# Kernel optimization log

Measured on AMD Instinct MI355X. Metric: run time of the kernel, lower is better.

The kernel has to match this reference:

```python
import jax, jax.numpy as jnp
import numpy as np

T, D, R, C, L = 4096, 512, 32, 32, 2  # time, input, trace, context, num_blocks
NEG_SLOPE = 0.01
EPS = 1e-5  # eqx LayerNorm default


def _layernorm(x, g, b):
    m = jnp.mean(x, -1, keepdims=True)
    v = jnp.var(x, -1, keepdims=True)
    return g * (x - m) * jax.lax.rsqrt(v + EPS) + b


def _ffa_scan(a, b, pre, s0, start):
    # a:[R], b:[C], pre:[T,R,C] real>=0, s0:[1,R,C] complex64, start:[T] bool
    ab = jax.lax.complex(jnp.broadcast_to(-jnp.abs(a)[:, None], (R, C)),
                         jnp.broadcast_to(b[None, :], (R, C)))  # log decay+rotation
    ts = jnp.concatenate([jnp.zeros((1,), jnp.float32), jnp.ones((T,), jnp.float32)])
    vals = jnp.concatenate([s0, pre.astype(jnp.complex64)], axis=0)  # [T+1,R,C]
    rst = jnp.concatenate([jnp.zeros((1,), bool), start])

    def op(l, r):
        tl, sl, dl = l
        tr, sr, dr = r
        decay = jnp.exp(ab[None, :, :] * tr[:, None, None])  # gamma^{t_r}
        s = jnp.where(dr[:, None, None], sr, sr + sl * decay)
        t = jnp.where(dr, tr, tl + tr)
        return (t, s, dl | dr)

    _, states, _ = jax.lax.associative_scan(op, (ts, vals, rst))
    return states[1:]  # [T,R,C]


def _forward(x, start_b, state_real, state_imag, Wt, Wc, a, b,
             W0, b0, g0, beta0, W1, b1, g1, beta1):
    h = x
    z = x
    for i in range(L):
        tr = h @ Wt[i].T  # [T,R]
        ct = h @ Wc[i].T  # [T,R] (source maps context proj to trace_size too; R==C)
        pre = jnp.abs(tr[:, :, None] * ct[:, None, :])  # [T,R,C] outer product
        pre = pre / (1e-8 + jnp.sum(pre, axis=(-2, -1), keepdims=True))
        s0 = jax.lax.complex(state_real[i], state_imag[i])  # [1,R,C]
        states = _ffa_scan(a[i], b[i], pre, s0, start_b)
        s = states.reshape(T, R * C)
        mag = jnp.log1p(jnp.abs(s))
        ang = jnp.angle(s)
        scaled = jnp.concatenate([mag * jnp.sin(ang), mag * jnp.cos(ang)], axis=-1)  # [T,2RC]
        z = jax.nn.leaky_relu(_layernorm(scaled @ W0[i].T + b0[i], g0[i], beta0[i]), NEG_SLOPE)
        z = jax.nn.leaky_relu(_layernorm(z @ W1[i].T + b1[i], g1[i], beta1[i]), NEG_SLOPE)
        h = h + z  # residual feeds next block; NSFFM returns last block's z
    return z


def setup_inputs() -> dict:
    key = jax.random.key(0)
    ks = jax.random.split(key, 8)
    x = jax.random.normal(ks[0], (T, D), jnp.float32)
    start = jax.random.randint(ks[1], (T,), 0, 2).astype(jnp.int32)
    next_done = jax.random.randint(ks[2], (T,), 0, 2).astype(jnp.int32)
    Wt = jax.random.normal(ks[3], (L, R, D), jnp.float32) / np.sqrt(D)
    Wc = jax.random.normal(ks[4], (L, R, D), jnp.float32) / np.sqrt(D)
    # ffa.init: a = linspace decays, b = log-spaced angular frequencies
    a = jnp.broadcast_to(jnp.linspace(1e-6, 0.5, R, dtype=jnp.float32)[None], (L, R)).copy()
    b = jnp.broadcast_to((2 * jnp.pi / jnp.exp(jnp.linspace(np.log(1.0), np.log(1024.0), C))).astype(jnp.float32)[None], (L, C)).copy()
    W0 = jax.random.normal(ks[5], (L, D, 2 * R * C), jnp.float32) * 0.01  # default_init scale=0.01
    W1 = jax.random.normal(ks[6], (L, D, D), jnp.float32) / np.sqrt(D)
    return {
        'x': x, 'start': start, 'next_done': next_done,
        'state_real': jnp.zeros((L, 1, R, C), jnp.float32),
        'state_imag': jnp.zeros((L, 1, R, C), jnp.float32),
        'Wt': Wt, 'Wc': Wc, 'a': a, 'b': b,
        'W0': W0, 'b0': jnp.zeros((L, D), jnp.float32),
        'g0': jnp.ones((L, D), jnp.float32), 'beta0': jnp.zeros((L, D), jnp.float32),
        'W1': W1, 'b1': jnp.zeros((L, D), jnp.float32),
        'g1': jnp.ones((L, D), jnp.float32), 'beta1': jnp.zeros((L, D), jnp.float32),
    }


def reference(x, start, next_done, state_real, state_imag, Wt, Wc, a, b,
              W0, b0, g0, beta0, W1, b1, g1, beta1):
    del next_done  # not used in the scan math (kept for interface parity)
    start_b = start.astype(bool)
    return _forward(x, start_b, state_real, state_imag, Wt, Wc, a, b,
                    W0, b0, g0, beta0, W1, b1, g1, beta1)
```

## Files before the change

kernel.cpp:

```cpp
#include <hip/hip_runtime.h>
#include <math.h>

#define TT 4096
#define DD 512
#define RR 32
#define CC 32
#define RC 1024
#define LL 2
#define CHUNK 32
#define NCHUNK 128
#define NEG_SLOPE 0.01f
#define LN_EPS 1e-5f

typedef __attribute__((ext_vector_type(8))) __bf16 bf16x8;
typedef __attribute__((ext_vector_type(4))) float f32x4;

__device__ __forceinline__ unsigned short f2bf(float f) {
    unsigned int u = __builtin_bit_cast(unsigned int, f);
    u += 0x7fffu + ((u >> 16) & 1u);
    return (unsigned short)(u >> 16);
}

#define NX4  524288
#define NW04 524288
#define NW14 131072
__global__ __launch_bounds__(256) void conv_all_kernel(const float4* __restrict__ x,
                                                       const float4* __restrict__ W0,
                                                       const float4* __restrict__ W1,
                                                       ushort4* __restrict__ xb,
                                                       ushort4* __restrict__ W0b,
                                                       ushort4* __restrict__ W1b) {
    int i = blockIdx.x * 256 + threadIdx.x;
    const float4* src; ushort4* dst; int j;
    if (i < NX4) { src = x; dst = xb; j = i; }
    else if (i < NX4 + NW04) { src = W0; dst = W0b; j = i - NX4; }
    else { src = W1; dst = W1b; j = i - NX4 - NW04; }
    float4 v = src[j];
    ushort4 o;
    o.x = f2bf(v.x); o.y = f2bf(v.y); o.z = f2bf(v.z); o.w = f2bf(v.w);
    dst[j] = o;
}

__global__ __launch_bounds__(256) void pack_wtc_kernel(const float* __restrict__ Wt,
                                                       const float* __restrict__ Wc,
                                                       ushort4* __restrict__ Wtc) {
    int i = blockIdx.x * 256 + threadIdx.x;
    int e = i * 4;
    int l = e >> 15;
    int r = (e >> 9) & 63;
    int k = e & 511;
    const float4 v = (r < 32)
        ? *(const float4*)&Wt[((size_t)l * 32 + r) * 512 + k]
        : *(const float4*)&Wc[((size_t)l * 32 + (r - 32)) * 512 + k];
    ushort4 o;
    o.x = f2bf(v.x); o.y = f2bf(v.y); o.z = f2bf(v.z); o.w = f2bf(v.w);
    Wtc[i] = o;
}

__global__ __launch_bounds__(256) void denom_reduce_kernel(const float* __restrict__ tcp,
                                                           float* __restrict__ tcabs) {
    int lrow = threadIdx.x >> 3;
    int q = threadIdx.x & 7;
    int row = blockIdx.x * 32 + lrow;
    size_t base = (size_t)row * 64 + q * 8;
    float v[8];
#pragma unroll
    for (int e = 0; e < 8; ++e) v[e] = 0.f;
#pragma unroll
    for (int z = 0; z < 4; ++z) {
        const float4* p = (const float4*)(tcp + (size_t)z * TT * 64 + base);
        float4 u0 = p[0], u1 = p[1];
        v[0] += u0.x; v[1] += u0.y; v[2] += u0.z; v[3] += u0.w;
        v[4] += u1.x; v[5] += u1.y; v[6] += u1.z; v[7] += u1.w;
    }
    float s = 0.f;
#pragma unroll
    for (int e = 0; e < 8; ++e) { v[e] = fabsf(v[e]); s += v[e]; }
    __shared__ float red[32][8];
    red[lrow][q] = s;
    __syncthreads();
    float str = red[lrow][0] + red[lrow][1] + red[lrow][2] + red[lrow][3];
    float stc = red[lrow][4] + red[lrow][5] + red[lrow][6] + red[lrow][7];
    float inv = 1.f / (1e-8f + str * stc);
    float scale = (q < 4) ? inv : 1.f;
    float4 o0 = make_float4(v[0] * scale, v[1] * scale, v[2] * scale, v[3] * scale);
    float4 o1 = make_float4(v[4] * scale, v[5] * scale, v[6] * scale, v[7] * scale);
    float4* dst = (float4*)(tcabs + base);
    dst[0] = o0; dst[1] = o1;
}

__global__ __launch_bounds__(256) void scan_pass1(const float* __restrict__ tcabs,
                                                  const int* __restrict__ start,
                                                  const float* __restrict__ a,
                                                  const float* __restrict__ b,
                                                  float4* __restrict__ ab4) {
    int tid = blockIdx.x * 256 + threadIdx.x;
    int rc = tid & (RC - 1);
    int chunk = tid >> 10;
    int r = rc >> 5, c = rc & 31;
    float e = expf(-fabsf(a[r]));
    float gr = e * cosf(b[c]);
    float gi = e * sinf(b[c]);
    float alr = 1.f, ali = 0.f, ber = 0.f, bei = 0.f;
    int t0 = chunk * CHUNK;
    for (int j = 0; j < CHUNK; ++j) {
        int t = t0 + j;
        float pre = tcabs[t * 64 + r] * tcabs[t * 64 + 32 + c];
        if (start[t]) {
            alr = 0.f; ali = 0.f; ber = pre; bei = 0.f;
        } else {
            float nbr = pre + gr * ber - gi * bei;
            float nbi =       gr * bei + gi * ber;
            float nar = gr * alr - gi * ali;
            float nai = gr * ali + gi * alr;
            ber = nbr; bei = nbi; alr = nar; ali = nai;
        }
    }
    ab4[chunk * RC + rc] = make_float4(alr, ali, ber, bei);
}

__global__ __launch_bounds__(256) void scan_combine(const float4* __restrict__ ab4,
                                                    const float* __restrict__ s0r,
                                                    const float* __restrict__ s0i,
                                                    float2* __restrict__ inc) {
    int rc = blockIdx.x * 256 + threadIdx.x;
    float sr = s0r[rc], si = s0i[rc];
    for (int kb = 0; kb < NCHUNK; kb += 8) {
        float4 buf[8];
#pragma unroll
        for (int u = 0; u < 8; ++u) buf[u] = ab4[(kb + u) * RC + rc];
#pragma unroll
        for (int u = 0; u < 8; ++u) {
            inc[(kb + u) * RC + rc] = make_float2(sr, si);
            float nsr = buf[u].z + buf[u].x * sr - buf[u].y * si;
            float nsi = buf[u].w + buf[u].x * si + buf[u].y * sr;
            sr = nsr; si = nsi;
        }
    }
}

__global__ __launch_bounds__(256) void scan_pass2(const float* __restrict__ tcabs,
                                                  const int* __restrict__ start,
                                                  const float* __restrict__ a,
                                                  const float* __restrict__ b,
                                                  const float2* __restrict__ inc,
                                                  unsigned short* __restrict__ scaled) {
    int tid = blockIdx.x * 256 + threadIdx.x;
    int rc = tid & (RC - 1);
    int chunk = tid >> 10;
    int r = rc >> 5, c = rc & 31;
    float e = expf(-fabsf(a[r]));
    float gr = e * cosf(b[c]);
    float gi = e * sinf(b[c]);
    float2 s = inc[chunk * RC + rc];
    float sr = s.x, si = s.y;
    int t0 = chunk * CHUNK;
    for (int j = 0; j < CHUNK; ++j) {
        int t = t0 + j;
        float pre = tcabs[t * 64 + r] * tcabs[t * 64 + 32 + c];
        if (start[t]) {
            sr = pre; si = 0.f;
        } else {
            float nsr = pre + gr * sr - gi * si;
            float nsi =       gr * si + gi * sr;
            sr = nsr; si = nsi;
        }
        float m = sqrtf(sr * sr + si * si);
        float mag = log1pf(m);
        float f = (m > 0.f) ? (mag / m) : 0.f;
        scaled[(size_t)t * 2048 + rc]        = f2bf(si * f);
        scaled[(size_t)t * 2048 + 1024 + rc] = f2bf(sr * f);
    }
}

template <int K, int N, int SPLITK>
__global__ __launch_bounds__(256) void gemm_bt_mfma(const unsigned short* __restrict__ A,
                                                    const unsigned short* __restrict__ B,
                                                    float* __restrict__ Cm) {
    __shared__ unsigned short As[128 * 32];
    __shared__ unsigned short Bs[64 * 32];
    const int tid = threadIdx.x;
    const int w = tid >> 6, lane = tid & 63;
    const int bm = blockIdx.y * 128, bn = blockIdx.x * 64;
    const int kbeg = blockIdx.z * (K / SPLITK);
    const int kend = kbeg + (K / SPLITK);
    const int wr = w >> 1, wc = w & 1;
    const int lr = lane >> 2;
    const int sl = lane & 3;
    const int swz_st = sl ^ ((lr >> 1) & 3);
    const size_t a_row0 = (size_t)(bm + w * 16 + lr);
    const size_t a_row1 = (size_t)(bm + 64 + w * 16 + lr);
    const size_t b_row  = (size_t)(bn + w * 16 + lr);
    const unsigned short* gA0 = A + a_row0 * K + sl * 8;
    const unsigned short* gA1 = A + a_row1 * K + sl * 8;
    const unsigned short* gB  = B + b_row  * K + sl * 8;
    const int wA0 = (w * 16 + lr) * 32 + swz_st * 8;
    const int wA1 = (64 + w * 16 + lr) * 32 + swz_st * 8;
    const int wB  = (w * 16 + lr) * 32 + swz_st * 8;
    const int fr = lane & 15;
    const int kslot = (lane >> 4) ^ ((fr >> 1) & 3);
    f32x4 acc[4][2] = {};

    uint4 va0 = *(const uint4*)(gA0 + kbeg);
    uint4 va1 = *(const uint4*)(gA1 + kbeg);
    uint4 vb  = *(const uint4*)(gB  + kbeg);
    for (int k0 = kbeg; k0 < kend; k0 += 32) {
        __syncthreads();
        *(uint4*)&As[wA0] = va0;
        *(uint4*)&As[wA1] = va1;
        *(uint4*)&Bs[wB]  = vb;
        __syncthreads();
        if (k0 + 32 < kend) {
            va0 = *(const uint4*)(gA0 + k0 + 32);
            va1 = *(const uint4*)(gA1 + k0 + 32);
            vb  = *(const uint4*)(gB  + k0 + 32);
        }
        bf16x8 af[4], bfr[2];
#pragma unroll
        for (int mi = 0; mi < 4; ++mi) {
            int row = wr * 64 + mi * 16 + fr;
            af[mi] = *(const bf16x8*)&As[row * 32 + kslot * 8];
        }
#pragma unroll
        for (int ni = 0; ni < 2; ++ni) {
            int row = wc * 32 + ni * 16 + fr;
            bfr[ni] = *(const bf16x8*)&Bs[row * 32 + kslot * 8];
        }
#pragma unroll
        for (int mi = 0; mi < 4; ++mi)
#pragma unroll
            for (int ni = 0; ni < 2; ++ni)
                acc[mi][ni] = __builtin_amdgcn_mfma_f32_16x16x32_bf16(
                    af[mi], bfr[ni], acc[mi][ni], 0, 0, 0);
    }
    float* Cz = Cm + (size_t)blockIdx.z * TT * N;
    const int ccol0 = bn + wc * 32 + fr;
    const int crow0 = bm + wr * 64 + (lane >> 4) * 4;
#pragma unroll
    for (int ni = 0; ni < 2; ++ni) {
        int col = ccol0 + ni * 16;
#pragma unroll
        for (int mi = 0; mi < 4; ++mi)
#pragma unroll
            for (int q = 0; q < 4; ++q)
                Cz[(size_t)(crow0 + mi * 16 + q) * N + col] = acc[mi][ni][q];
    }
}

__global__ __launch_bounds__(256) void ln_lrelu_kernel(const float* __restrict__ y0,
                                                       const float* __restrict__ y1,
                                                       const float* __restrict__ badd,
                                                       const float* __restrict__ g,
                                                       const float* __restrict__ be,
                                                       unsigned short* __restrict__ zb,
                                                       const float* __restrict__ res,
                                                       unsigned short* __restrict__ hbf,
                                                       float* __restrict__ fout) {
    int t = blockIdx.x;
    int tid = threadIdx.x;
    size_t base = (size_t)t * 512;
    float v0 = y0[base + tid] + y1[base + tid] + badd[tid];
    float v1 = y0[base + 256 + tid] + y1[base + 256 + tid] + badd[256 + tid];
    float s = v0 + v1, ss = v0 * v0 + v1 * v1;
#pragma unroll
    for (int o = 32; o > 0; o >>= 1) {
        s  += __shfl_down(s, o);
        ss += __shfl_down(ss, o);
    }
    __shared__ float sh[8];
    __shared__ float mrs[2];
    int wid = tid >> 6, lane = tid & 63;
    if (lane == 0) { sh[wid] = s; sh[4 + wid] = ss; }
    __syncthreads();
    if (tid == 0) {
        float S = sh[0] + sh[1] + sh[2] + sh[3];
        float SS = sh[4] + sh[5] + sh[6] + sh[7];
        float m = S * (1.f / 512.f);
        float var = SS * (1.f / 512.f) - m * m;
        mrs[0] = m;
        mrs[1] = rsqrtf(var + LN_EPS);
    }
    __syncthreads();
    float m = mrs[0], rs = mrs[1];
    float z0 = g[tid] * (v0 - m) * rs + be[tid];
    float z1 = g[256 + tid] * (v1 - m) * rs + be[256 + tid];
    z0 = (z0 > 0.f) ? z0 : NEG_SLOPE * z0;
    z1 = (z1 > 0.f) ? z1 : NEG_SLOPE * z1;
    if (zb)   { zb[base + tid] = f2bf(z0); zb[base + 256 + tid] = f2bf(z1); }
    if (hbf) {
        float h0 = (res ? res[base + tid] : 0.f) + z0;
        float h1 = (res ? res[base + 256 + tid] : 0.f) + z1;
        hbf[base + tid] = f2bf(h0);
        hbf[base + 256 + tid] = f2bf(h1);
    }
    if (fout) { fout[base + tid] = z0; fout[base + 256 + tid] = z1; }
}

extern "C" void kernel_launch(void* const* d_in, const int* in_sizes, int n_in,
                              void* d_out, int out_size, void* d_ws, size_t ws_size,
                              hipStream_t stream) {
    const float* x     = (const float*)d_in[0];
    const int*   start = (const int*)d_in[1];
    const float* s0r = (const float*)d_in[3];
    const float* s0i = (const float*)d_in[4];
    const float* Wt  = (const float*)d_in[5];
    const float* Wc  = (const float*)d_in[6];
    const float* a   = (const float*)d_in[7];
    const float* b   = (const float*)d_in[8];
    const float* W0  = (const float*)d_in[9];
    const float* b0  = (const float*)d_in[10];
    const float* g0  = (const float*)d_in[11];
    const float* be0 = (const float*)d_in[12];
    const float* W1  = (const float*)d_in[13];
    const float* b1  = (const float*)d_in[14];
    const float* g1  = (const float*)d_in[15];
    const float* be1 = (const float*)d_in[16];
    float* out = (float*)d_out;
    float* ws  = (float*)d_ws;

    float* p = ws;
    float* tcp    = p; p += 1048576;
    float* tcabs  = p; p += 262144;
    float4* ab4   = (float4*)p; p += 524288;
    float2* inc   = (float2*)p; p += 262144;
    unsigned short* scaled = (unsigned short*)p; p += 4194304;
    float* ybufp  = p; p += 4194304;
    unsigned short* zbuf_bf = (unsigned short*)p; p += 1048576;
    unsigned short* x_bf    = (unsigned short*)p; p += 1048576;
    unsigned short* h_bf    = (unsigned short*)p; p += 1048576;
    unsigned short* Wtcbf   = (unsigned short*)p; p += 32768;
    unsigned short* W0bf    = (unsigned short*)p; p += 1048576;
    unsigned short* W1bf    = (unsigned short*)p; p += 262144;

    conv_all_kernel<<<(NX4 + NW04 + NW14) / 256, 256, 0, stream>>>(
        (const float4*)x, (const float4*)W0, (const float4*)W1,
        (ushort4*)x_bf, (ushort4*)W0bf, (ushort4*)W1bf);
    pack_wtc_kernel<<<64, 256, 0, stream>>>(Wt, Wc, (ushort4*)Wtcbf);

    for (int i = 0; i < LL; ++i) {
        const unsigned short* hb = (i == 0) ? x_bf : h_bf;
        gemm_bt_mfma<512, 64, 4><<<dim3(1, 32, 4), 256, 0, stream>>>(
            hb, Wtcbf + (size_t)i * 64 * 512, tcp);
        denom_reduce_kernel<<<128, 256, 0, stream>>>(tcp, tcabs);
        scan_pass1<<<NCHUNK * RC / 256, 256, 0, stream>>>(
            tcabs, start, a + i * RR, b + i * CC, ab4);
        scan_combine<<<4, 256, 0, stream>>>(ab4, s0r + i * RC, s0i + i * RC, inc);
        scan_pass2<<<NCHUNK * RC / 256, 256, 0, stream>>>(
            tcabs, start, a + i * RR, b + i * CC, inc, scaled);
        gemm_bt_mfma<2048, 512, 2><<<dim3(8, 32, 2), 256, 0, stream>>>(
            scaled, W0bf + (size_t)i * 512 * 2048, ybufp);
        ln_lrelu_kernel<<<TT, 256, 0, stream>>>(
            ybufp, ybufp + (size_t)TT * 512, b0 + i * DD, g0 + i * DD, be0 + i * DD,
            zbuf_bf, nullptr, nullptr, nullptr);
        gemm_bt_mfma<512, 512, 2><<<dim3(8, 32, 2), 256, 0, stream>>>(
            zbuf_bf, W1bf + (size_t)i * 512 * 512, ybufp);
        ln_lrelu_kernel<<<TT, 256, 0, stream>>>(
            ybufp, ybufp + (size_t)TT * 512, b1 + i * DD, g1 + i * DD, be1 + i * DD,
            nullptr,
            (i < LL - 1) ? x : nullptr,
            (i < LL - 1) ? h_bf : nullptr,
            (i == LL - 1) ? out : nullptr);
    }
}
```

Measured before the change: 214.8 us.

## Fuse projection with denominator, fold scan combine into pass2, widen GEMM K-tile

The two setup conversion kernels become one launch. The projection GEMM now computes the abs and row-normalisation directly in its epilogue, with no split-K and no separate reduce kernel. The serial scan_combine kernel is removed: each pass2 block recomputes its chunk's incoming state by folding all prior chunk summaries, which trades a launch and a serial pass for redundant O(chunk) work per block. The generic GEMM moves from a 32-wide to a 64-wide K tile with a new XOR swizzle, giving fewer barriers per K and more MFMAs per sync.

After: 324.9 us. 51.2% more time.

```diff
diff --git a/kernel.cpp b/kernel.cpp
--- a/kernel.cpp
+++ b/kernel.cpp
@@ -24,69 +24,137 @@
 #define NX4  524288
 #define NW04 524288
 #define NW14 131072
-__global__ __launch_bounds__(256) void conv_all_kernel(const float4* __restrict__ x,
-                                                       const float4* __restrict__ W0,
-                                                       const float4* __restrict__ W1,
-                                                       ushort4* __restrict__ xb,
-                                                       ushort4* __restrict__ W0b,
-                                                       ushort4* __restrict__ W1b) {
+#define NCV  (NX4 + NW04 + NW14)
+#define NPK  16384
+__global__ __launch_bounds__(256) void setup_kernel(const float4* __restrict__ x,
+                                                    const float4* __restrict__ W0,
+                                                    const float4* __restrict__ W1,
+                                                    const float* __restrict__ Wt,
+                                                    const float* __restrict__ Wc,
+                                                    ushort4* __restrict__ xb,
+                                                    ushort4* __restrict__ W0b,
+                                                    ushort4* __restrict__ W1b,
+                                                    ushort4* __restrict__ Wtc) {
     int i = blockIdx.x * 256 + threadIdx.x;
-    const float4* src; ushort4* dst; int j;
-    if (i < NX4) { src = x; dst = xb; j = i; }
-    else if (i < NX4 + NW04) { src = W0; dst = W0b; j = i - NX4; }
-    else { src = W1; dst = W1b; j = i - NX4 - NW04; }
-    float4 v = src[j];
+    float4 v;
+    ushort4* dst;
+    int j;
+    if (i < NCV) {
+        const float4* src;
+        if (i < NX4) { src = x; dst = xb; j = i; }
+        else if (i < NX4 + NW04) { src = W0; dst = W0b; j = i - NX4; }
+        else { src = W1; dst = W1b; j = i - NX4 - NW04; }
+        v = src[j];
+    } else {
+        int ii = i - NCV;
+        if (ii >= NPK) return;
+        int e = ii * 4;
+        int l = e >> 15;
+        int r = (e >> 9) & 63;
+        int k = e & 511;
+        v = (r < 32) ? *(const float4*)&Wt[((size_t)l * 32 + r) * 512 + k]
+                     : *(const float4*)&Wc[((size_t)l * 32 + (r - 32)) * 512 + k];
+        dst = Wtc; j = ii;
+    }
     ushort4 o;
     o.x = f2bf(v.x); o.y = f2bf(v.y); o.z = f2bf(v.z); o.w = f2bf(v.w);
     dst[j] = o;
 }
 
-__global__ __launch_bounds__(256) void pack_wtc_kernel(const float* __restrict__ Wt,
-                                                       const float* __restrict__ Wc,
-                                                       ushort4* __restrict__ Wtc) {
-    int i = blockIdx.x * 256 + threadIdx.x;
-    int e = i * 4;
-    int l = e >> 15;
-    int r = (e >> 9) & 63;
-    int k = e & 511;
-    const float4 v = (r < 32)
-        ? *(const float4*)&Wt[((size_t)l * 32 + r) * 512 + k]
-        : *(const float4*)&Wc[((size_t)l * 32 + (r - 32)) * 512 + k];
-    ushort4 o;
-    o.x = f2bf(v.x); o.y = f2bf(v.y); o.z = f2bf(v.z); o.w = f2bf(v.w);
-    Wtc[i] = o;
-}
-
-__global__ __launch_bounds__(256) void denom_reduce_kernel(const float* __restrict__ tcp,
-                                                           float* __restrict__ tcabs) {
-    int lrow = threadIdx.x >> 3;
-    int q = threadIdx.x & 7;
-    int row = blockIdx.x * 32 + lrow;
-    size_t base = (size_t)row * 64 + q * 8;
-    float v[8];
-#pragma unroll
-    for (int e = 0; e < 8; ++e) v[e] = 0.f;
-#pragma unroll
-    for (int z = 0; z < 4; ++z) {
-        const float4* p = (const float4*)(tcp + (size_t)z * TT * 64 + base);
-        float4 u0 = p[0], u1 = p[1];
-        v[0] += u0.x; v[1] += u0.y; v[2] += u0.z; v[3] += u0.w;
-        v[4] += u1.x; v[5] += u1.y; v[6] += u1.z; v[7] += u1.w;
-    }
-    float s = 0.f;
-#pragma unroll
-    for (int e = 0; e < 8; ++e) { v[e] = fabsf(v[e]); s += v[e]; }
-    __shared__ float red[32][8];
-    red[lrow][q] = s;
+__global__ __launch_bounds__(256) void proj_denom_kernel(const unsigned short* __restrict__ A,
+                                                         const unsigned short* __restrict__ B,
+                                                         float* __restrict__ tcabs) {
+    __shared__ __align__(16) unsigned short As[128 * 64];
+    __shared__ __align__(16) unsigned short Bs[64 * 64];
+    __shared__ float sums[128][2];
+    const int tid = threadIdx.x;
+    const int w = tid >> 6, lane = tid & 63;
+    const int bm = blockIdx.y * 128;
+    const int wr = w >> 1, wc = w & 1;
+    const int fr = lane & 15, hi = lane >> 4;
+    const int K = 512;
+    const unsigned short* ga[4]; int wa[4];
+    const unsigned short* gb[2]; int wb[2];
+#pragma unroll
+    for (int u = 0; u < 4; ++u) {
+        int vid = u * 256 + tid;
+        int row = vid >> 3, k8 = vid & 7;
+        ga[u] = A + (size_t)(bm + row) * K + k8 * 8;
+        wa[u] = row * 64 + ((k8 ^ (row & 7)) * 8);
+    }
+#pragma unroll
+    for (int u = 0; u < 2; ++u) {
+        int vid = u * 256 + tid;
+        int row = vid >> 3, k8 = vid & 7;
+        gb[u] = B + (size_t)row * K + k8 * 8;
+        wb[u] = row * 64 + ((k8 ^ (row & 7)) * 8);
+    }
+    f32x4 acc[4][2] = {};
+    uint4 pa[4], pb[2];
+#pragma unroll
+    for (int u = 0; u < 4; ++u) pa[u] = *(const uint4*)ga[u];
+#pragma unroll
+    for (int u = 0; u < 2; ++u) pb[u] = *(const uint4*)gb[u];
+    for (int k0 = 0; k0 < K; k0 += 64) {
+        __syncthreads();
+#pragma unroll
+        for (int u = 0; u < 4; ++u) *(uint4*)&As[wa[u]] = pa[u];
+#pragma unroll
+        for (int u = 0; u < 2; ++u) *(uint4*)&Bs[wb[u]] = pb[u];
+        __syncthreads();
+        if (k0 + 64 < K) {
+#pragma unroll
+            for (int u = 0; u < 4; ++u) pa[u] = *(const uint4*)(ga[u] + k0 + 64);
+#pragma unroll
+            for (int u = 0; u < 2; ++u) pb[u] = *(const uint4*)(gb[u] + k0 + 64);
+        }
+#pragma unroll
+        for (int kk = 0; kk < 2; ++kk) {
+            const int ks = kk * 4 + hi;
+            bf16x8 af[4], bfv[2];
+#pragma unroll
+            for (int mi = 0; mi < 4; ++mi) {
+                int row = wr * 64 + mi * 16 + fr;
+                af[mi] = *(const bf16x8*)&As[row * 64 + ((ks ^ (row & 7)) * 8)];
+            }
+#pragma unroll
+            for (int ni = 0; ni < 2; ++ni) {
+                int row = wc * 32 + ni * 16 + fr;
+                bfv[ni] = *(const bf16x8*)&Bs[row * 64 + ((ks ^ (row & 7)) * 8)];
+            }
+#pragma unroll
+            for (int mi = 0; mi < 4; ++mi)
+#pragma unroll
+                for (int ni = 0; ni < 2; ++ni)
+                    acc[mi][ni] = __builtin_amdgcn_mfma_f32_16x16x32_bf16(
+                        af[mi], bfv[ni], acc[mi][ni], 0, 0, 0);
+        }
+    }
+#pragma unroll
+    for (int mi = 0; mi < 4; ++mi)
+#pragma unroll
+        for (int q = 0; q < 4; ++q) {
+            float v = fabsf(acc[mi][0][q]) + fabsf(acc[mi][1][q]);
+            v += __shfl_xor(v, 1);
+            v += __shfl_xor(v, 2);
+            v += __shfl_xor(v, 4);
+            v += __shfl_xor(v, 8);
+            if (fr == 0) sums[wr * 64 + mi * 16 + hi * 4 + q][wc] = v;
+        }
     __syncthreads();
-    float str = red[lrow][0] + red[lrow][1] + red[lrow][2] + red[lrow][3];
-    float stc = red[lrow][4] + red[lrow][5] + red[lrow][6] + red[lrow][7];
-    float inv = 1.f / (1e-8f + str * stc);
-    float scale = (q < 4) ? inv : 1.f;
-    float4 o0 = make_float4(v[0] * scale, v[1] * scale, v[2] * scale, v[3] * scale);
-    float4 o1 = make_float4(v[4] * scale, v[5] * scale, v[6] * scale, v[7] * scale);
-    float4* dst = (float4*)(tcabs + base);
-    dst[0] = o0; dst[1] = o1;
+#pragma unroll
+    for (int mi = 0; mi < 4; ++mi)
+#pragma unroll
+        for (int q = 0; q < 4; ++q) {
+            int rl = wr * 64 + mi * 16 + hi * 4 + q;
+            float inv = 1.f / (1e-8f + sums[rl][0] * sums[rl][1]);
+            float scale = (wc == 0) ? inv : 1.f;
+#pragma unroll
+            for (int ni = 0; ni < 2; ++ni) {
+                int col = wc * 32 + ni * 16 + fr;
+                tcabs[(size_t)(bm + rl) * 64 + col] = fabsf(acc[mi][ni][q]) * scale;
+            }
+        }
 }
 
 __global__ __launch_bounds__(256) void scan_pass1(const float* __restrict__ tcabs,
@@ -119,44 +187,43 @@
     ab4[chunk * RC + rc] = make_float4(alr, ali, ber, bei);
 }
 
-__global__ __launch_bounds__(256) void scan_combine(const float4* __restrict__ ab4,
-                                                    const float* __restrict__ s0r,
-                                                    const float* __restrict__ s0i,
-                                                    float2* __restrict__ inc) {
-    int rc = blockIdx.x * 256 + threadIdx.x;
-    float sr = s0r[rc], si = s0i[rc];
-    for (int kb = 0; kb < NCHUNK; kb += 8) {
-        float4 buf[8];
-#pragma unroll
-        for (int u = 0; u < 8; ++u) buf[u] = ab4[(kb + u) * RC + rc];
-#pragma unroll
-        for (int u = 0; u < 8; ++u) {
-            inc[(kb + u) * RC + rc] = make_float2(sr, si);
-            float nsr = buf[u].z + buf[u].x * sr - buf[u].y * si;
-            float nsi = buf[u].w + buf[u].x * si + buf[u].y * sr;
-            sr = nsr; si = nsi;
-        }
-    }
-}
-
-__global__ __launch_bounds__(256) void scan_pass2(const float* __restrict__ tcabs,
-                                                  const int* __restrict__ start,
-                                                  const float* __restrict__ a,
-                                                  const float* __restrict__ b,
-                                                  const float2* __restrict__ inc,
-                                                  unsigned short* __restrict__ scaled) {
-    int tid = blockIdx.x * 256 + threadIdx.x;
-    int rc = tid & (RC - 1);
-    int chunk = tid >> 10;
+__global__ __launch_bounds__(256) void scan_pass2f(const float* __restrict__ tcabs,
+                                                   const float4* __restrict__ ab4,
+                                                   const int* __restrict__ start,
+                                                   const float* __restrict__ a,
+                                                   const float* __restrict__ b,
+                                                   const float* __restrict__ s0r,
+                                                   const float* __restrict__ s0i,
+                                                   unsigned short* __restrict__ scaled) {
+    int bx = blockIdx.x;
+    int chunk = bx >> 2;
+    int rc = (bx & 3) * 256 + threadIdx.x;
     int r = rc >> 5, c = rc & 31;
     float e = expf(-fabsf(a[r]));
     float gr = e * cosf(b[c]);
     float gi = e * sinf(b[c]);
-    float2 s = inc[chunk * RC + rc];
-    float sr = s.x, si = s.y;
+    float sr = s0r[rc], si = s0i[rc];
+    int j = 0;
+    for (; j + 8 <= chunk; j += 8) {
+        float4 buf[8];
+#pragma unroll
+        for (int u = 0; u < 8; ++u) buf[u] = ab4[(j + u) * RC + rc];
+#pragma unroll
+        for (int u = 0; u < 8; ++u) {
+            float nsr = buf[u].z + buf[u].x * sr - buf[u].y * si;
+            float nsi = buf[u].w + buf[u].x * si + buf[u].y * sr;
+            sr = nsr; si = nsi;
+        }
+    }
+    for (; j < chunk; ++j) {
+        float4 ab = ab4[j * RC + rc];
+        float nsr = ab.z + ab.x * sr - ab.y * si;
+        float nsi = ab.w + ab.x * si + ab.y * sr;
+        sr = nsr; si = nsi;
+    }
     int t0 = chunk * CHUNK;
-    for (int j = 0; j < CHUNK; ++j) {
-        int t = t0 + j;
+    for (int jj = 0; jj < CHUNK; ++jj) {
+        int t = t0 + jj;
         float pre = tcabs[t * 64 + r] * tcabs[t * 64 + 32 + c];
         if (start[t]) {
             sr = pre; si = 0.f;
@@ -177,65 +244,75 @@
 __global__ __launch_bounds__(256) void gemm_bt_mfma(const unsigned short* __restrict__ A,
                                                     const unsigned short* __restrict__ B,
                                                     float* __restrict__ Cm) {
-    __shared__ unsigned short As[128 * 32];
-    __shared__ unsigned short Bs[64 * 32];
+    __shared__ __align__(16) unsigned short As[128 * 64];
+    __shared__ __align__(16) unsigned short Bs[64 * 64];
     const int tid = threadIdx.x;
     const int w = tid >> 6, lane = tid & 63;
     const int bm = blockIdx.y * 128, bn = blockIdx.x * 64;
     const int kbeg = blockIdx.z * (K / SPLITK);
     const int kend = kbeg + (K / SPLITK);
     const int wr = w >> 1, wc = w & 1;
-    const int lr = lane >> 2;
-    const int sl = lane & 3;
-    const int swz_st = sl ^ ((lr >> 1) & 3);
-    const size_t a_row0 = (size_t)(bm + w * 16 + lr);
-    const size_t a_row1 = (size_t)(bm + 64 + w * 16 + lr);
-    const size_t b_row  = (size_t)(bn + w * 16 + lr);
-    const unsigned short* gA0 = A + a_row0 * K + sl * 8;
-    const unsigned short* gA1 = A + a_row1 * K + sl * 8;
-    const unsigned short* gB  = B + b_row  * K + sl * 8;
-    const int wA0 = (w * 16 + lr) * 32 + swz_st * 8;
-    const int wA1 = (64 + w * 16 + lr) * 32 + swz_st * 8;
-    const int wB  = (w * 16 + lr) * 32 + swz_st * 8;
-    const int fr = lane & 15;
-    const int kslot = (lane >> 4) ^ ((fr >> 1) & 3);
+    const int fr = lane & 15, hi = lane >> 4;
+    const unsigned short* ga[4]; int wa[4];
+    const unsigned short* gb[2]; int wb[2];
+#pragma unroll
+    for (int u = 0; u < 4; ++u) {
+        int vid = u * 256 + tid;
+        int row = vid >> 3, k8 = vid & 7;
+        ga[u] = A + (size_t)(bm + row) * K + k8 * 8;
+        wa[u] = row * 64 + ((k8 ^ (row & 7)) * 8);
+    }
+#pragma unroll
+    for (int u = 0; u < 2; ++u) {
+        int vid = u * 256 + tid;
+        int row = vid >> 3, k8 = vid & 7;
+        gb[u] = B + (size_t)(bn + row) * K + k8 * 8;
+        wb[u] = row * 64 + ((k8 ^ (row & 7)) * 8);
+    }
     f32x4 acc[4][2] = {};
-
-    uint4 va0 = *(const uint4*)(gA0 + kbeg);
-    uint4 va1 = *(const uint4*)(gA1 + kbeg);
-    uint4 vb  = *(const uint4*)(gB  + kbeg);
-    for (int k0 = kbeg; k0 < kend; k0 += 32) {
+    uint4 pa[4], pb[2];
+#pragma unroll
+    for (int u = 0; u < 4; ++u) pa[u] = *(const uint4*)(ga[u] + kbeg);
+#pragma unroll
+    for (int u = 0; u < 2; ++u) pb[u] = *(const uint4*)(gb[u] + kbeg);
+    for (int k0 = kbeg; k0 < kend; k0 += 64) {
         __syncthreads();
-        *(uint4*)&As[wA0] = va0;
-        *(uint4*)&As[wA1] = va1;
-        *(uint4*)&Bs[wB]  = vb;
+#pragma unroll
+        for (int u = 0; u < 4; ++u) *(uint4*)&As[wa[u]] = pa[u];
+#pragma unroll
+        for (int u = 0; u < 2; ++u) *(uint4*)&Bs[wb[u]] = pb[u];
         __syncthreads();
-        if (k0 + 32 < kend) {
-            va0 = *(const uint4*)(gA0 + k0 + 32);
-            va1 = *(const uint4*)(gA1 + k0 + 32);
-            vb  = *(const uint4*)(gB  + k0 + 32);
-        }
-        bf16x8 af[4], bfr[2];
-#pragma unroll
-        for (int mi = 0; mi < 4; ++mi) {
-            int row = wr * 64 + mi * 16 + fr;
-            af[mi] = *(const bf16x8*)&As[row * 32 + kslot * 8];
-        }
-#pragma unroll
-        for (int ni = 0; ni < 2; ++ni) {
-            int row = wc * 32 + ni * 16 + fr;
-            bfr[ni] = *(const bf16x8*)&Bs[row * 32 + kslot * 8];
-        }
-#pragma unroll
-        for (int mi = 0; mi < 4; ++mi)
-#pragma unroll
-            for (int ni = 0; ni < 2; ++ni)
-                acc[mi][ni] = __builtin_amdgcn_mfma_f32_16x16x32_bf16(
-                    af[mi], bfr[ni], acc[mi][ni], 0, 0, 0);
+        if (k0 + 64 < kend) {
+#pragma unroll
+            for (int u = 0; u < 4; ++u) pa[u] = *(const uint4*)(ga[u] + k0 + 64);
+#pragma unroll
+            for (int u = 0; u < 2; ++u) pb[u] = *(const uint4*)(gb[u] + k0 + 64);
+        }
+#pragma unroll
+        for (int kk = 0; kk < 2; ++kk) {
+            const int ks = kk * 4 + hi;
+            bf16x8 af[4], bfv[2];
+#pragma unroll
+            for (int mi = 0; mi < 4; ++mi) {
+                int row = wr * 64 + mi * 16 + fr;
+                af[mi] = *(const bf16x8*)&As[row * 64 + ((ks ^ (row & 7)) * 8)];
+            }
+#pragma unroll
+            for (int ni = 0; ni < 2; ++ni) {
+                int row = wc * 32 + ni * 16 + fr;
+                bfv[ni] = *(const bf16x8*)&Bs[row * 64 + ((ks ^ (row & 7)) * 8)];
+            }
+#pragma unroll
+            for (int mi = 0; mi < 4; ++mi)
+#pragma unroll
+                for (int ni = 0; ni < 2; ++ni)
+                    acc[mi][ni] = __builtin_amdgcn_mfma_f32_16x16x32_bf16(
+                        af[mi], bfv[ni], acc[mi][ni], 0, 0, 0);
+        }
     }
     float* Cz = Cm + (size_t)blockIdx.z * TT * N;
     const int ccol0 = bn + wc * 32 + fr;
-    const int crow0 = bm + wr * 64 + (lane >> 4) * 4;
+    const int crow0 = bm + wr * 64 + hi * 4;
 #pragma unroll
     for (int ni = 0; ni < 2; ++ni) {
         int col = ccol0 + ni * 16;
@@ -319,10 +396,8 @@
     float* ws  = (float*)d_ws;
 
     float* p = ws;
-    float* tcp    = p; p += 1048576;
     float* tcabs  = p; p += 262144;
     float4* ab4   = (float4*)p; p += 524288;
-    float2* inc   = (float2*)p; p += 262144;
     unsigned short* scaled = (unsigned short*)p; p += 4194304;
     float* ybufp  = p; p += 4194304;
     unsigned short* zbuf_bf = (unsigned short*)p; p += 1048576;
@@ -332,21 +407,19 @@
     unsigned short* W0bf    = (unsigned short*)p; p += 1048576;
     unsigned short* W1bf    = (unsigned short*)p; p += 262144;
 
-    conv_all_kernel<<<(NX4 + NW04 + NW14) / 256, 256, 0, stream>>>(
-        (const float4*)x, (const float4*)W0, (const float4*)W1,
-        (ushort4*)x_bf, (ushort4*)W0bf, (ushort4*)W1bf);
-    pack_wtc_kernel<<<64, 256, 0, stream>>>(Wt, Wc, (ushort4*)Wtcbf);
+    setup_kernel<<<(NCV + NPK + 255) / 256, 256, 0, stream>>>(
+        (const float4*)x, (const float4*)W0, (const float4*)W1, Wt, Wc,
+        (ushort4*)x_bf, (ushort4*)W0bf, (ushort4*)W1bf, (ushort4*)Wtcbf);
 
     for (int i = 0; i < LL; ++i) {
         const unsigned short* hb = (i == 0) ? x_bf : h_bf;
-        gemm_bt_mfma<512, 64, 4><<<dim3(1, 32, 4), 256, 0, stream>>>(
-            hb, Wtcbf + (size_t)i * 64 * 512, tcp);
-        denom_reduce_kernel<<<128, 256, 0, stream>>>(tcp, tcabs);
+        proj_denom_kernel<<<dim3(1, 32), 256, 0, stream>>>(
+            hb, Wtcbf + (size_t)i * 64 * 512, tcabs);
         scan_pass1<<<NCHUNK * RC / 256, 256, 0, stream>>>(
             tcabs, start, a + i * RR, b + i * CC, ab4);
-        scan_combine<<<4, 256, 0, stream>>>(ab4, s0r + i * RC, s0i + i * RC, inc);
-        scan_pass2<<<NCHUNK * RC / 256, 256, 0, stream>>>(
-            tcabs, start, a + i * RR, b + i * CC, inc, scaled);
+        scan_pass2f<<<NCHUNK * 4, 256, 0, stream>>>(
+            tcabs, ab4, start, a + i * RR, b + i * CC,
+            s0r + i * RC, s0i + i * RC, scaled);
         gemm_bt_mfma<2048, 512, 2><<<dim3(8, 32, 2), 256, 0, stream>>>(
             scaled, W0bf + (size_t)i * 512 * 2048, ybufp);
         ln_lrelu_kernel<<<TT, 256, 0, stream>>>(
```
